# Kernel optimization log

Measured on AMD Instinct MI355X. Metric: run time of the kernel, lower is better.

Reference implementation:

```python
import jax, jax.numpy as jnp
import numpy as np

HEAD = 4
EPS = 1e-12


def _l2norm(x, axis):
    # torch F.normalize: x / max(||x||_2, eps)
    return x / jnp.maximum(jnp.linalg.norm(x, axis=axis, keepdims=True), EPS)


def setup_inputs() -> dict:
    key = jax.random.key(0)
    ks = jax.random.split(key, 12)
    n, t, c, h, w = 2, 7, 96, 96, 96
    inp = {
        "curr_feat": jax.random.normal(ks[0], (n, c, h, w), jnp.float32),
        "index_feat_set_s1": jax.random.normal(ks[1], (n, t, c, h, w), jnp.float32),
        "anchor_feat": jax.random.normal(ks[2], (n, c, h, w), jnp.float32),
        "sparse_feat_set_s1": jax.random.normal(ks[3], (n, t, c, h, w), jnp.float32),
        "sparse_feat_set_s2": jax.random.normal(ks[4], (n, t, c, h, w), jnp.float32),
        "sparse_feat_set_s3": jax.random.normal(ks[5], (n, t, c, h, w), jnp.float32),
        # absolute pixel coordinates (x,y interleaved per frame), mostly in-bounds
        # with a little overshoot to exercise zeros padding of grid_sample
        "location_feat": jax.random.uniform(ks[6], (n, t * 2, h, w), jnp.float32, minval=-2.0, maxval=float(w) + 1.0),
        "proj_w": 0.02 * jax.random.normal(ks[7], (c, c), jnp.float32),
        "proj_b": jnp.zeros((c,), jnp.float32),
        "fusion_w": 0.02 * jax.random.normal(ks[8], (c, 3 * c), jnp.float32),
        "fusion_b": jnp.zeros((c,), jnp.float32),
    }
    return inp


def reference(curr_feat, index_feat_set_s1, anchor_feat, sparse_feat_set_s1,
              sparse_feat_set_s2, sparse_feat_set_s3, location_feat,
              proj_w, proj_b, fusion_w, fusion_b):
    n, c, h, w = anchor_feat.shape
    t = sparse_feat_set_s1.shape[1]
    hd = c // HEAD
    hw = h * w

    # ---- flow-guided nearest grid_sample (align_corners=True, zeros pad) ----
    loc = location_feat.reshape(n, t, 2, h, w)  # (n,t,2,h,w): [x, y] pixel coords
    gx = 2.0 * loc[:, :, 0] / max(w - 1, 1) - 1.0
    gy = 2.0 * loc[:, :, 1] / max(h - 1, 1) - 1.0
    ix = jnp.round((gx + 1.0) * 0.5 * (w - 1))  # nearest (round-half-even, as torch)
    iy = jnp.round((gy + 1.0) * 0.5 * (h - 1))
    valid = (ix >= 0) & (ix <= w - 1) & (iy >= 0) & (iy <= h - 1)
    lin = (jnp.clip(iy, 0, h - 1).astype(jnp.int32) * w
           + jnp.clip(ix, 0, w - 1).astype(jnp.int32)).reshape(n, t, 1, hw)
    vmask = valid.reshape(n, t, 1, hw)

    def sample(f):  # f: (n,t,c,h,w) -> gathered (n,t,c,hw)
        g = jnp.take_along_axis(f.reshape(n, t, c, hw), lin, axis=3)
        return jnp.where(vmask, g, 0.0)

    samp1 = sample(sparse_feat_set_s1)
    samp2 = sample(sparse_feat_set_s2)
    samp3 = sample(sparse_feat_set_s3)
    sampi = sample(index_feat_set_s1)

    # ---- per-pixel multi-head max-correlation over t frames ----
    # queries: normalize over full channel dim c BEFORE splitting into heads
    q = _l2norm(curr_feat.reshape(n, c, hw).transpose(0, 2, 1), -1).reshape(n, hw, HEAD, hd)
    k = _l2norm(sampi.transpose(0, 3, 1, 2), -1).reshape(n, hw, t, HEAD, hd)
    scores = jnp.einsum('npthd,nphd->npht', k, q)  # scale == 1.0 in mode='max'
    corr_soft = jnp.max(scores, axis=3)     # (n,hw,head)
    corr_index = jnp.argmax(scores, axis=3)  # (n,hw,head), first-max like torch

    soft_img = jnp.broadcast_to(corr_soft[..., None], (n, hw, HEAD, hd)) \
                  .reshape(n, h, w, c).transpose(0, 3, 1, 2)  # (n,c,h,w)
    idx = jnp.broadcast_to(corr_index[..., None], (n, hw, HEAD, hd)) \
             .reshape(n, hw, c).transpose(0, 2, 1)[:, None]  # (n,1,c,hw)

    def pick(samp):  # select winning frame per (channel-group, pixel)
        return jnp.take_along_axis(samp, idx, axis=1)[:, 0].reshape(n, c, h, w)

    cat = jnp.concatenate([pick(samp1), pick(samp2), pick(samp3)], axis=1)  # (n,3c,h,w)
    out = jnp.einsum('ndhw,cd->nchw', cat, fusion_w) + fusion_b[None, :, None, None]
    out = out * soft_img
    out = jnp.einsum('nchw,dc->ndhw', out, proj_w) + proj_b[None, :, None, None]
    return out + anchor_feat
```

## Files before the change

### kernel.cpp

```cpp
#include <hip/hip_runtime.h>
#include <hip/hip_bf16.h>

#define N_    2
#define T_    7
#define C_    96
#define H_    96
#define W_    96
#define HW_   9216
#define HEAD_ 4
#define HD_   24
#define C3_   288
#define P_    16
#define QP_   100
#define CATP_ 292
#define NBLK_ (N_ * (HW_ / P_))
#define PLANES_ 14
#define CHUNK_  64
#define NCHUNK_ 144

typedef unsigned int u32;

__device__ __forceinline__ float bits2f(u32 b) {
    union { u32 u; float f; } x; x.u = b; return x.f;
}

__device__ __forceinline__ unsigned short f2bf(float f) {
    union { __hip_bfloat16 h; unsigned short s; } u;
    u.h = __float2bfloat16(f);
    return u.s;
}

template<bool BF16>
__device__ __forceinline__ float ld1(const void* p, int i) {
    if constexpr (BF16) return bits2f(((u32)((const unsigned short*)p)[i]) << 16);
    else                return ((const float*)p)[i];
}

template<bool BF16>
__device__ __forceinline__ void ld4w(const void* p, int i, float w[4]) {
    if constexpr (BF16) {
        const uint2 u = ((const uint2*)p)[i >> 2];
        w[0] = bits2f(u.x << 16);
        w[1] = bits2f(u.x & 0xFFFF0000u);
        w[2] = bits2f(u.y << 16);
        w[3] = bits2f(u.y & 0xFFFF0000u);
    } else {
        const float4 v = *((const float4*)((const float*)p + i));
        w[0] = v.x; w[1] = v.y; w[2] = v.z; w[3] = v.w;
    }
}

template<bool BF16>
__device__ __forceinline__ void st4w(void* p, int i, const float v[4]) {
    if constexpr (BF16) {
        uint2 w;
        w.x = (u32)f2bf(v[0]) | ((u32)f2bf(v[1]) << 16);
        w.y = (u32)f2bf(v[2]) | ((u32)f2bf(v[3]) << 16);
        ((uint2*)p)[i >> 2] = w;
    } else {
        *((float4*)((float*)p + i)) = make_float4(v[0], v[1], v[2], v[3]);
    }
}

__device__ __forceinline__ bool block_detect_bf16(const u32* __restrict__ w,
                                                  int tid, int* s_flag) {
    if (tid < 64) {
        u32 x = w[tid];
        u32 f = x & 0x7FFFu;
        int inwin = (f >= 0x3A00u) && (f <= 0x4200u);
        unsigned long long m = __ballot(inwin);
        if (tid == 0) *s_flag = (__popcll(m) >= 40) ? 1 : 0;
    }
    __syncthreads();
    return *s_flag != 0;
}

template<bool BF16>
__device__ __forceinline__ void transp_body(const void* __restrict__ src,
                                            void* __restrict__ dst,
                                            int bx, int tid, char* tileraw) {
    const int pl = bx / NCHUNK_;
    const int x0 = (bx - pl * NCHUNK_) * CHUNK_;
    if constexpr (BF16) {
        unsigned short (*tile)[CHUNK_ + 2] = (unsigned short (*)[CHUNK_ + 2])tileraw;
        const unsigned short* s = (const unsigned short*)src;
        unsigned short* d = (unsigned short*)dst;
        for (int i = tid; i < C_ * (CHUNK_ / 4); i += 256) {
            int ch = i >> 4, xq = i & 15;
            const ushort4 v = *((const ushort4*)(s + (pl * C_ + ch) * HW_ + x0 + 4 * xq));
            tile[ch][4 * xq + 0] = v.x; tile[ch][4 * xq + 1] = v.y;
            tile[ch][4 * xq + 2] = v.z; tile[ch][4 * xq + 3] = v.w;
        }
        __syncthreads();
        for (int i = tid; i < CHUNK_ * (C_ / 4); i += 256) {
            int p = i / 24, cq = i - p * 24;
            ushort4 v;
            v.x = tile[4 * cq + 0][p]; v.y = tile[4 * cq + 1][p];
            v.z = tile[4 * cq + 2][p]; v.w = tile[4 * cq + 3][p];
            *((ushort4*)(d + (pl * HW_ + x0 + p) * C_ + 4 * cq)) = v;
        }
    } else {
        float (*tile)[CHUNK_ + 1] = (float (*)[CHUNK_ + 1])tileraw;
        const float* s = (const float*)src;
        float* d = (float*)dst;
        for (int i = tid; i < C_ * (CHUNK_ / 4); i += 256) {
            int ch = i >> 4, xq = i & 15;
            const float4 v = *((const float4*)(s + (pl * C_ + ch) * HW_ + x0 + 4 * xq));
            tile[ch][4 * xq + 0] = v.x; tile[ch][4 * xq + 1] = v.y;
            tile[ch][4 * xq + 2] = v.z; tile[ch][4 * xq + 3] = v.w;
        }
        __syncthreads();
        for (int i = tid; i < CHUNK_ * (C_ / 4); i += 256) {
            int p = i / 24, cq = i - p * 24;
            float4 v;
            v.x = tile[4 * cq + 0][p]; v.y = tile[4 * cq + 1][p];
            v.z = tile[4 * cq + 2][p]; v.w = tile[4 * cq + 3][p];
            *((float4*)(d + (pl * HW_ + x0 + p) * C_ + 4 * cq)) = v;
        }
    }
}

__global__ __launch_bounds__(256) void transp_kernel(
    const void* __restrict__ idxf, void* __restrict__ dst,
    const u32* __restrict__ detect_src)
{
    __shared__ __align__(16) char tileraw[C_ * (CHUNK_ + 1) * 4];
    __shared__ int s_flag;
    const int tid = threadIdx.x;
    const bool bf = block_detect_bf16(detect_src, tid, &s_flag);
    if (bf) transp_body<true >(idxf, dst, blockIdx.x, tid, tileraw);
    else    transp_body<false>(idxf, dst, blockIdx.x, tid, tileraw);
}

template<bool BF16, int MODE>
__device__ __forceinline__ void traj_body(
    const void* __restrict__ curr, const void* __restrict__ idxf,
    const void* __restrict__ anchor, const void* __restrict__ s1,
    const void* __restrict__ s2, const void* __restrict__ s3,
    const void* __restrict__ loc, const void* __restrict__ pw,
    const void* __restrict__ pb, const void* __restrict__ fw,
    const void* __restrict__ fb, void* __restrict__ outp,
    const void* __restrict__ kT,
    float* s_u, float (*s_mid)[QP_], int (*s_lin)[P_], float (*s_red)[8],
    float (*s_best)[HEAD_], int (*s_bidx)[HEAD_], float* s_inv)
{
#define S_Q(pp, ch)  s_u[(pp) * QP_ + (ch)]
#define S_K(pp, ch)  s_u[P_ * QP_ + (pp) * QP_ + (ch)]
#define S_CAT(pp, d) s_u[(pp) * CATP_ + (d)]

    const int tid = threadIdx.x;
    const int b  = blockIdx.x;
    const int nn = b / (HW_ / P_);
    const int p0 = (b - nn * (HW_ / P_)) * P_;

    if (tid < T_ * P_) {
        int t = tid / P_, pp = tid - t * P_;
        int p = p0 + pp;
        float x = ld1<BF16>(loc, (nn * 2 * T_ + 2 * t    ) * HW_ + p);
        float y = ld1<BF16>(loc, (nn * 2 * T_ + 2 * t + 1) * HW_ + p);
        float gx = 2.0f * x / 95.0f - 1.0f;
        float gy = 2.0f * y / 95.0f - 1.0f;
        float fx = (gx + 1.0f) * 0.5f * 95.0f;
        float fy = (gy + 1.0f) * 0.5f * 95.0f;
        float ix = rintf(fx), iy = rintf(fy);
        bool v = (ix >= 0.0f) && (ix <= 95.0f) && (iy >= 0.0f) && (iy <= 95.0f);
        s_lin[t][pp] = v ? ((int)iy * W_ + (int)ix) : -1;
    }
    if (tid >= 128 && tid < 128 + P_ * HEAD_) {
        int q = tid - 128;
        s_best[q >> 2][q & 3] = -3.0e38f; s_bidx[q >> 2][q & 3] = 0;
    }

    for (int i = tid; i < C_ * (P_ / 4); i += 256) {
        int ch = i >> 2, pq = i & 3;
        float w[4];
        ld4w<BF16>(curr, (nn * C_ + ch) * HW_ + p0 + 4 * pq, w);
        S_Q(4 * pq + 0, ch) = w[0]; S_Q(4 * pq + 1, ch) = w[1];
        S_Q(4 * pq + 2, ch) = w[2]; S_Q(4 * pq + 3, ch) = w[3];
    }
    __syncthreads();

    if (tid < P_ * 8) {
        int pp = tid >> 3, j = tid & 7;
        float s = 0.f;
        #pragma unroll
        for (int k = 0; k < 12; ++k) { float v = S_Q(pp, j * 12 + k); s += v * v; }
        s_red[pp][j] = s;
    }
    __syncthreads();
    if (tid < P_) {
        float s = 0.f;
        #pragma unroll
        for (int j = 0; j < 8; ++j) s += s_red[tid][j];
        s_inv[tid] = 1.0f / fmaxf(sqrtf(s), 1e-12f);
    }
    __syncthreads();
    for (int i = tid; i < C_ * P_; i += 256) {
        int pp = i & (P_ - 1), ch = i >> 4;
        S_Q(pp, ch) *= s_inv[pp];
    }

    for (int t = 0; t < T_; ++t) {
        __syncthreads();
        if constexpr (MODE >= 1) {
            for (int i = tid; i < 24 * P_; i += 256) {
                int pp = i / 24, j = i - pp * 24;
                int lin = s_lin[t][pp];
                float w[4] = {0.f, 0.f, 0.f, 0.f};
                if (lin >= 0) ld4w<BF16>(kT, ((nn * T_ + t) * HW_ + lin) * C_ + 4 * j, w);
                *((float4*)&S_K(pp, 4 * j)) = make_float4(w[0], w[1], w[2], w[3]);
            }
        } else {
            for (int i = tid; i < C_ * P_; i += 256) {
                int ch = i / P_, pp = i - ch * P_;
                int lin = s_lin[t][pp];
                S_K(pp, ch) = (lin >= 0) ? ld1<BF16>(idxf, ((nn * T_ + t) * C_ + ch) * HW_ + lin) : 0.0f;
            }
        }
        __syncthreads();
        if (tid < P_ * 8) {
            int pp = tid >> 3, j = tid & 7;
            float s = 0.f;
            #pragma unroll
            for (int k = 0; k < 12; ++k) { float v = S_K(pp, j * 12 + k); s += v * v; }
            s_red[pp][j] = s;
        }
        __syncthreads();
        if (tid < P_) {
            float s = 0.f;
            #pragma unroll
            for (int j = 0; j < 8; ++j) s += s_red[tid][j];
            s_inv[tid] = 1.0f / fmaxf(sqrtf(s), 1e-12f);
        }
        __syncthreads();
        if (tid < P_ * HEAD_) {
            int pp = tid >> 2, h = tid & 3;
            float s = 0.f;
            #pragma unroll
            for (int dq = 0; dq < 6; ++dq) {
                const float4 kv = *((const float4*)&S_K(pp, h * HD_ + 4 * dq));
                const float4 qv = *((const float4*)&S_Q(pp, h * HD_ + 4 * dq));
                s += kv.x * qv.x; s += kv.y * qv.y; s += kv.z * qv.z; s += kv.w * qv.w;
            }
            s *= s_inv[pp];
            if (s > s_best[pp][h]) { s_best[pp][h] = s; s_bidx[pp][h] = t; }
        }
    }
    __syncthreads();

    for (int i = tid; i < C3_ * P_; i += 256) {
        int pp = i / C3_, d = i - pp * C3_;
        int set = d / C_, ch = d - set * C_;
        int h = ch / HD_;
        int bt = s_bidx[pp][h];
        int lin = s_lin[bt][pp];
        float v = 0.f;
        if (lin >= 0) {
            const void* sp = (set == 0) ? s1 : (set == 1) ? s2 : s3;
            v = ld1<BF16>(sp, ((nn * T_ + bt) * C_ + ch) * HW_ + lin);
        }
        S_CAT(pp, d) = v;
    }
    __syncthreads();

    if (tid < 96) {
        const int cq = tid >> 2, pq = tid & 3;
        const int co0 = cq * 4, px0 = pq * 4;
        float acc[4][4];
        #pragma unroll
        for (int r = 0; r < 4; ++r)
            #pragma unroll
            for (int k = 0; k < 4; ++k) acc[r][k] = 0.f;
        for (int d = 0; d < C3_; d += 4) {
            float4 cv[4];
            #pragma unroll
            for (int k = 0; k < 4; ++k) cv[k] = *((const float4*)&S_CAT(px0 + k, d));
            #pragma unroll
            for (int r = 0; r < 4; ++r) {
                float w[4]; ld4w<BF16>(fw, (co0 + r) * C3_ + d, w);
                #pragma unroll
                for (int k = 0; k < 4; ++k)
                    acc[r][k] += w[0] * cv[k].x + w[1] * cv[k].y + w[2] * cv[k].z + w[3] * cv[k].w;
            }
        }
        const int hh = co0 / HD_;
        #pragma unroll
        for (int r = 0; r < 4; ++r) {
            float fbv = ld1<BF16>(fb, co0 + r);
            #pragma unroll
            for (int k = 0; k < 4; ++k)
                s_mid[px0 + k][co0 + r] = (acc[r][k] + fbv) * s_best[px0 + k][hh];
        }
    }
    __syncthreads();

    if (tid < 96) {
        const int dq = tid >> 2, pq = tid & 3;
        const int do0 = dq * 4, px0 = pq * 4;
        float acc[4][4];
        #pragma unroll
        for (int r = 0; r < 4; ++r)
            #pragma unroll
            for (int k = 0; k < 4; ++k) acc[r][k] = 0.f;
        for (int c = 0; c < C_; c += 4) {
            float4 mv[4];
            #pragma unroll
            for (int k = 0; k < 4; ++k) mv[k] = *((const float4*)&s_mid[px0 + k][c]);
            #pragma unroll
            for (int r = 0; r < 4; ++r) {
                float w[4]; ld4w<BF16>(pw, (do0 + r) * C_ + c, w);
                #pragma unroll
                for (int k = 0; k < 4; ++k)
                    acc[r][k] += w[0] * mv[k].x + w[1] * mv[k].y + w[2] * mv[k].z + w[3] * mv[k].w;
            }
        }
        #pragma unroll
        for (int r = 0; r < 4; ++r) {
            float pbv = ld1<BF16>(pb, do0 + r);
            float av[4];
            ld4w<BF16>(anchor, (nn * C_ + do0 + r) * HW_ + p0 + px0, av);
            float res[4];
            #pragma unroll
            for (int k = 0; k < 4; ++k) res[k] = acc[r][k] + pbv + av[k];
            st4w<BF16>(outp, (nn * C_ + do0 + r) * HW_ + p0 + px0, res);
        }
    }
#undef S_Q
#undef S_K
#undef S_CAT
}

template<int MODE>
__global__ __launch_bounds__(256) void traj_main(
    const void* __restrict__ curr, const void* __restrict__ idxf,
    const void* __restrict__ anchor, const void* __restrict__ s1,
    const void* __restrict__ s2, const void* __restrict__ s3,
    const void* __restrict__ loc, const void* __restrict__ pw,
    const void* __restrict__ pb, const void* __restrict__ fw,
    const void* __restrict__ fb, void* __restrict__ outp,
    const void* __restrict__ kT)
{
    __shared__ __align__(16) float s_u[P_ * CATP_];
    __shared__ __align__(16) float s_mid[P_][QP_];
    __shared__ int   s_lin[T_][P_];
    __shared__ float s_red[P_][8];
    __shared__ float s_best[P_][HEAD_];
    __shared__ int   s_bidx[P_][HEAD_];
    __shared__ float s_inv[P_];
    __shared__ int   s_flag;

    const bool bf = block_detect_bf16((const u32*)curr, threadIdx.x, &s_flag);
    if (bf) traj_body<true,  MODE>(curr, idxf, anchor, s1, s2, s3, loc, pw, pb, fw, fb,
                                   outp, kT, s_u, s_mid, s_lin, s_red, s_best, s_bidx, s_inv);
    else    traj_body<false, MODE>(curr, idxf, anchor, s1, s2, s3, loc, pw, pb, fw, fb,
                                   outp, kT, s_u, s_mid, s_lin, s_red, s_best, s_bidx, s_inv);
}

extern "C" void kernel_launch(void* const* d_in, const int* in_sizes, int n_in,
                              void* d_out, int out_size, void* d_ws, size_t ws_size,
                              hipStream_t stream) {
    (void)in_sizes; (void)n_in; (void)out_size;
    const unsigned long long SZB = (unsigned long long)N_ * T_ * HW_ * C_ * 4ull;
    void* kT = d_ws;
    const int mode = (ws_size >= SZB) ? 1 : 0;

    dim3 grid(NBLK_), block(256);
    if (mode == 1) {
        transp_kernel<<<dim3(PLANES_ * NCHUNK_), 256, 0, stream>>>(d_in[1], kT, (const u32*)d_in[0]);
        traj_main<1><<<grid, block, 0, stream>>>(d_in[0], d_in[1], d_in[2], d_in[3], d_in[4],
                                                 d_in[5], d_in[6], d_in[7], d_in[8], d_in[9],
                                                 d_in[10], d_out, kT);
    } else {
        traj_main<0><<<grid, block, 0, stream>>>(d_in[0], d_in[1], d_in[2], d_in[3], d_in[4],
                                                 d_in[5], d_in[6], d_in[7], d_in[8], d_in[9],
                                                 d_in[10], d_out, kT);
    }
}
```

Measured before the change: 332.9 us.

## Gather all frames at once and restructure per-block work with 512 threads

The main kernel now loads the sampled key features for all seven frames in one batched phase instead of looping frame by frame with several barriers each. Norms, scores and the argmax are computed in parallel over frames and then reduced. The block size goes from 256 to 512 threads and the pixel tile from 16 to 12, with the fusion and projection matmuls remapped so each thread handles one pixel and four output channels. The goal is more memory-level parallelism and far fewer serialized barriers, at the cost of more shared memory per block and less register reuse of weights across pixels.

```diff
diff --git a/kernel.cpp b/kernel.cpp
--- a/kernel.cpp
+++ b/kernel.cpp
@@ -10,7 +10,7 @@
 #define HEAD_ 4
 #define HD_   24
 #define C3_   288
-#define P_    16
+#define P_    12
 #define QP_   100
 #define CATP_ 292
 #define NBLK_ (N_ * (HW_ / P_))
@@ -51,15 +51,9 @@
 }
 
 template<bool BF16>
-__device__ __forceinline__ void st4w(void* p, int i, const float v[4]) {
-    if constexpr (BF16) {
-        uint2 w;
-        w.x = (u32)f2bf(v[0]) | ((u32)f2bf(v[1]) << 16);
-        w.y = (u32)f2bf(v[2]) | ((u32)f2bf(v[3]) << 16);
-        ((uint2*)p)[i >> 2] = w;
-    } else {
-        *((float4*)((float*)p + i)) = make_float4(v[0], v[1], v[2], v[3]);
-    }
+__device__ __forceinline__ void st1(void* p, int i, float v) {
+    if constexpr (BF16) ((unsigned short*)p)[i] = f2bf(v);
+    else                ((float*)p)[i] = v;
 }
 
 __device__ __forceinline__ bool block_detect_bf16(const u32* __restrict__ w,
@@ -141,12 +135,13 @@
     const void* __restrict__ pb, const void* __restrict__ fw,
     const void* __restrict__ fb, void* __restrict__ outp,
     const void* __restrict__ kT,
-    float* s_u, float (*s_mid)[QP_], int (*s_lin)[P_], float (*s_red)[8],
-    float (*s_best)[HEAD_], int (*s_bidx)[HEAD_], float* s_inv)
+    float* s_q, float* s_ku, float (*s_mid)[QP_], int (*s_lin)[P_],
+    float* s_red, float* s_invq, float (*s_invk)[P_],
+    float (*s_score)[P_][HEAD_], float (*s_best)[HEAD_], int (*s_gbase)[HEAD_])
 {
-#define S_Q(pp, ch)  s_u[(pp) * QP_ + (ch)]
-#define S_K(pp, ch)  s_u[P_ * QP_ + (pp) * QP_ + (ch)]
-#define S_CAT(pp, d) s_u[(pp) * CATP_ + (d)]
+#define S_Q(pp, ch)     s_q[(pp) * QP_ + (ch)]
+#define S_K(t, pp, ch)  s_ku[((t) * P_ + (pp)) * QP_ + (ch)]
+#define S_CAT(pp, d)    s_ku[(pp) * CATP_ + (d)]
 
     const int tid = threadIdx.x;
     const int b  = blockIdx.x;
@@ -166,163 +161,160 @@
         bool v = (ix >= 0.0f) && (ix <= 95.0f) && (iy >= 0.0f) && (iy <= 95.0f);
         s_lin[t][pp] = v ? ((int)iy * W_ + (int)ix) : -1;
     }
-    if (tid >= 128 && tid < 128 + P_ * HEAD_) {
-        int q = tid - 128;
-        s_best[q >> 2][q & 3] = -3.0e38f; s_bidx[q >> 2][q & 3] = 0;
-    }
-
-    for (int i = tid; i < C_ * (P_ / 4); i += 256) {
-        int ch = i >> 2, pq = i & 3;
+    __syncthreads();
+
+    for (int i = tid; i < C_ * (P_ / 4); i += 512) {
+        int ch = i / (P_ / 4), pq = i - ch * (P_ / 4);
         float w[4];
         ld4w<BF16>(curr, (nn * C_ + ch) * HW_ + p0 + 4 * pq, w);
         S_Q(4 * pq + 0, ch) = w[0]; S_Q(4 * pq + 1, ch) = w[1];
         S_Q(4 * pq + 2, ch) = w[2]; S_Q(4 * pq + 3, ch) = w[3];
     }
-    __syncthreads();
-
-    if (tid < P_ * 8) {
-        int pp = tid >> 3, j = tid & 7;
+    if constexpr (MODE >= 1) {
+        for (int i = tid; i < T_ * P_ * 24; i += 512) {
+            int t = i / (P_ * 24), rem = i - t * (P_ * 24);
+            int pp = rem / 24, j = rem - pp * 24;
+            int lin = s_lin[t][pp];
+            float w[4] = {0.f, 0.f, 0.f, 0.f};
+            if (lin >= 0) ld4w<BF16>(kT, ((nn * T_ + t) * HW_ + lin) * C_ + 4 * j, w);
+            *((float4*)&S_K(t, pp, 4 * j)) = make_float4(w[0], w[1], w[2], w[3]);
+        }
+    } else {
+        for (int i = tid; i < T_ * C_ * P_; i += 512) {
+            int t = i / (C_ * P_), rem = i - t * (C_ * P_);
+            int ch = rem / P_, pp = rem - ch * P_;
+            int lin = s_lin[t][pp];
+            S_K(t, pp, ch) = (lin >= 0) ? ld1<BF16>(idxf, ((nn * T_ + t) * C_ + ch) * HW_ + lin) : 0.0f;
+        }
+    }
+    __syncthreads();
+
+    for (int i = tid; i < P_ * 8 + T_ * P_ * 8; i += 512) {
+        if (i < P_ * 8) {
+            int pp = i >> 3, j = i & 7;
+            float s = 0.f;
+            #pragma unroll
+            for (int k = 0; k < 12; ++k) { float v = S_Q(pp, j * 12 + k); s += v * v; }
+            s_red[pp * 8 + j] = s;
+        } else {
+            int idx = i - P_ * 8;
+            int t = idx / (P_ * 8), rem = idx - t * (P_ * 8);
+            int pp = rem >> 3, j = rem & 7;
+            float s = 0.f;
+            #pragma unroll
+            for (int k = 0; k < 12; ++k) { float v = S_K(t, pp, j * 12 + k); s += v * v; }
+            s_red[P_ * 8 + (t * P_ + pp) * 8 + j] = s;
+        }
+    }
+    __syncthreads();
+
+    if (tid < P_ + T_ * P_) {
+        if (tid < P_) {
+            float s = 0.f;
+            #pragma unroll
+            for (int j = 0; j < 8; ++j) s += s_red[tid * 8 + j];
+            s_invq[tid] = 1.0f / fmaxf(sqrtf(s), 1e-12f);
+        } else {
+            int idx = tid - P_;
+            int t = idx / P_, pp = idx - t * P_;
+            float s = 0.f;
+            #pragma unroll
+            for (int j = 0; j < 8; ++j) s += s_red[P_ * 8 + (t * P_ + pp) * 8 + j];
+            s_invk[t][pp] = 1.0f / fmaxf(sqrtf(s), 1e-12f);
+        }
+    }
+    __syncthreads();
+
+    for (int i = tid; i < P_ * 24; i += 512) {
+        int pp = i / 24, chq = i - pp * 24;
+        float4* p4 = (float4*)&S_Q(pp, 4 * chq);
+        float4 v = *p4;
+        float iv = s_invq[pp];
+        v.x *= iv; v.y *= iv; v.z *= iv; v.w *= iv;
+        *p4 = v;
+    }
+    __syncthreads();
+
+    for (int i = tid; i < T_ * P_ * HEAD_; i += 512) {
+        int t = i / (P_ * HEAD_), rem = i - t * (P_ * HEAD_);
+        int pp = rem >> 2, h = rem & 3;
         float s = 0.f;
         #pragma unroll
-        for (int k = 0; k < 12; ++k) { float v = S_Q(pp, j * 12 + k); s += v * v; }
-        s_red[pp][j] = s;
-    }
-    __syncthreads();
-    if (tid < P_) {
-        float s = 0.f;
+        for (int dq = 0; dq < 6; ++dq) {
+            const float4 kv = *((const float4*)&S_K(t, pp, h * HD_ + 4 * dq));
+            const float4 qv = *((const float4*)&S_Q(pp, h * HD_ + 4 * dq));
+            s += kv.x * qv.x; s += kv.y * qv.y; s += kv.z * qv.z; s += kv.w * qv.w;
+        }
+        s *= s_invk[t][pp];
+        s_score[t][pp][h] = s;
+    }
+    __syncthreads();
+
+    if (tid < P_ * HEAD_) {
+        int pp = tid >> 2, h = tid & 3;
+        float best = -3.0e38f; int bidx = 0;
         #pragma unroll
-        for (int j = 0; j < 8; ++j) s += s_red[tid][j];
-        s_inv[tid] = 1.0f / fmaxf(sqrtf(s), 1e-12f);
-    }
-    __syncthreads();
-    for (int i = tid; i < C_ * P_; i += 256) {
-        int pp = i & (P_ - 1), ch = i >> 4;
-        S_Q(pp, ch) *= s_inv[pp];
-    }
-
-    for (int t = 0; t < T_; ++t) {
-        __syncthreads();
-        if constexpr (MODE >= 1) {
-            for (int i = tid; i < 24 * P_; i += 256) {
-                int pp = i / 24, j = i - pp * 24;
-                int lin = s_lin[t][pp];
-                float w[4] = {0.f, 0.f, 0.f, 0.f};
-                if (lin >= 0) ld4w<BF16>(kT, ((nn * T_ + t) * HW_ + lin) * C_ + 4 * j, w);
-                *((float4*)&S_K(pp, 4 * j)) = make_float4(w[0], w[1], w[2], w[3]);
-            }
-        } else {
-            for (int i = tid; i < C_ * P_; i += 256) {
-                int ch = i / P_, pp = i - ch * P_;
-                int lin = s_lin[t][pp];
-                S_K(pp, ch) = (lin >= 0) ? ld1<BF16>(idxf, ((nn * T_ + t) * C_ + ch) * HW_ + lin) : 0.0f;
-            }
-        }
-        __syncthreads();
-        if (tid < P_ * 8) {
-            int pp = tid >> 3, j = tid & 7;
-            float s = 0.f;
-            #pragma unroll
-            for (int k = 0; k < 12; ++k) { float v = S_K(pp, j * 12 + k); s += v * v; }
-            s_red[pp][j] = s;
-        }
-        __syncthreads();
-        if (tid < P_) {
-            float s = 0.f;
-            #pragma unroll
-            for (int j = 0; j < 8; ++j) s += s_red[tid][j];
-            s_inv[tid] = 1.0f / fmaxf(sqrtf(s), 1e-12f);
-        }
-        __syncthreads();
-        if (tid < P_ * HEAD_) {
-            int pp = tid >> 2, h = tid & 3;
-            float s = 0.f;
-            #pragma unroll
-            for (int dq = 0; dq < 6; ++dq) {
-                const float4 kv = *((const float4*)&S_K(pp, h * HD_ + 4 * dq));
-                const float4 qv = *((const float4*)&S_Q(pp, h * HD_ + 4 * dq));
-                s += kv.x * qv.x; s += kv.y * qv.y; s += kv.z * qv.z; s += kv.w * qv.w;
-            }
-            s *= s_inv[pp];
-            if (s > s_best[pp][h]) { s_best[pp][h] = s; s_bidx[pp][h] = t; }
-        }
-    }
-    __syncthreads();
-
-    for (int i = tid; i < C3_ * P_; i += 256) {
+        for (int t = 0; t < T_; ++t) {
+            float v = s_score[t][pp][h];
+            if (v > best) { best = v; bidx = t; }
+        }
+        s_best[pp][h] = best;
+        int lin = s_lin[bidx][pp];
+        s_gbase[pp][h] = (lin >= 0) ? ((nn * T_ + bidx) * C_ * HW_ + lin) : -1;
+    }
+    __syncthreads();
+
+    for (int i = tid; i < C3_ * P_; i += 512) {
         int pp = i / C3_, d = i - pp * C3_;
         int set = d / C_, ch = d - set * C_;
-        int h = ch / HD_;
-        int bt = s_bidx[pp][h];
-        int lin = s_lin[bt][pp];
+        int gb = s_gbase[pp][ch / HD_];
         float v = 0.f;
-        if (lin >= 0) {
+        if (gb >= 0) {
             const void* sp = (set == 0) ? s1 : (set == 1) ? s2 : s3;
-            v = ld1<BF16>(sp, ((nn * T_ + bt) * C_ + ch) * HW_ + lin);
+            v = ld1<BF16>(sp, gb + ch * HW_);
         }
         S_CAT(pp, d) = v;
     }
     __syncthreads();
 
-    if (tid < 96) {
-        const int cq = tid >> 2, pq = tid & 3;
-        const int co0 = cq * 4, px0 = pq * 4;
-        float acc[4][4];
+    if (tid < 24 * P_) {
+        const int cq = tid / P_, px = tid - cq * P_;
+        const int co0 = cq * 4;
+        float acc[4] = {0.f, 0.f, 0.f, 0.f};
+        for (int d = 0; d < C3_; d += 4) {
+            const float4 cv = *((const float4*)&S_CAT(px, d));
+            #pragma unroll
+            for (int r = 0; r < 4; ++r) {
+                float w[4]; ld4w<BF16>(fw, (co0 + r) * C3_ + d, w);
+                acc[r] += w[0] * cv.x + w[1] * cv.y + w[2] * cv.z + w[3] * cv.w;
+            }
+        }
+        const int hh = co0 / HD_;
+        float soft = s_best[px][hh];
         #pragma unroll
         for (int r = 0; r < 4; ++r)
-            #pragma unroll
-            for (int k = 0; k < 4; ++k) acc[r][k] = 0.f;
-        for (int d = 0; d < C3_; d += 4) {
-            float4 cv[4];
-            #pragma unroll
-            for (int k = 0; k < 4; ++k) cv[k] = *((const float4*)&S_CAT(px0 + k, d));
+            s_mid[px][co0 + r] = (acc[r] + ld1<BF16>(fb, co0 + r)) * soft;
+    }
+    __syncthreads();
+
+    if (tid < 24 * P_) {
+        const int dq = tid / P_, px = tid - dq * P_;
+        const int do0 = dq * 4;
+        float acc[4] = {0.f, 0.f, 0.f, 0.f};
+        for (int c = 0; c < C_; c += 4) {
+            const float4 mv = *((const float4*)&s_mid[px][c]);
             #pragma unroll
             for (int r = 0; r < 4; ++r) {
-                float w[4]; ld4w<BF16>(fw, (co0 + r) * C3_ + d, w);
-                #pragma unroll
-                for (int k = 0; k < 4; ++k)
-                    acc[r][k] += w[0] * cv[k].x + w[1] * cv[k].y + w[2] * cv[k].z + w[3] * cv[k].w;
+                float w[4]; ld4w<BF16>(pw, (do0 + r) * C_ + c, w);
+                acc[r] += w[0] * mv.x + w[1] * mv.y + w[2] * mv.z + w[3] * mv.w;
             }
         }
-        const int hh = co0 / HD_;
+        int p = p0 + px;
         #pragma unroll
         for (int r = 0; r < 4; ++r) {
-            float fbv = ld1<BF16>(fb, co0 + r);
-            #pragma unroll
-            for (int k = 0; k < 4; ++k)
-                s_mid[px0 + k][co0 + r] = (acc[r][k] + fbv) * s_best[px0 + k][hh];
-        }
-    }
-    __syncthreads();
-
-    if (tid < 96) {
-        const int dq = tid >> 2, pq = tid & 3;
-        const int do0 = dq * 4, px0 = pq * 4;
-        float acc[4][4];
-        #pragma unroll
-        for (int r = 0; r < 4; ++r)
-            #pragma unroll
-            for (int k = 0; k < 4; ++k) acc[r][k] = 0.f;
-        for (int c = 0; c < C_; c += 4) {
-            float4 mv[4];
-            #pragma unroll
-            for (int k = 0; k < 4; ++k) mv[k] = *((const float4*)&s_mid[px0 + k][c]);
-            #pragma unroll
-            for (int r = 0; r < 4; ++r) {
-                float w[4]; ld4w<BF16>(pw, (do0 + r) * C_ + c, w);
-                #pragma unroll
-                for (int k = 0; k < 4; ++k)
-                    acc[r][k] += w[0] * mv[k].x + w[1] * mv[k].y + w[2] * mv[k].z + w[3] * mv[k].w;
-            }
-        }
-        #pragma unroll
-        for (int r = 0; r < 4; ++r) {
-            float pbv = ld1<BF16>(pb, do0 + r);
-            float av[4];
-            ld4w<BF16>(anchor, (nn * C_ + do0 + r) * HW_ + p0 + px0, av);
-            float res[4];
-            #pragma unroll
-            for (int k = 0; k < 4; ++k) res[k] = acc[r][k] + pbv + av[k];
-            st4w<BF16>(outp, (nn * C_ + do0 + r) * HW_ + p0 + px0, res);
+            float res = acc[r] + ld1<BF16>(pb, do0 + r)
+                      + ld1<BF16>(anchor, (nn * C_ + do0 + r) * HW_ + p);
+            st1<BF16>(outp, (nn * C_ + do0 + r) * HW_ + p, res);
         }
     }
 #undef S_Q
@@ -331,7 +323,7 @@
 }
 
 template<int MODE>
-__global__ __launch_bounds__(256) void traj_main(
+__global__ __launch_bounds__(512, 6) void traj_main(
     const void* __restrict__ curr, const void* __restrict__ idxf,
     const void* __restrict__ anchor, const void* __restrict__ s1,
     const void* __restrict__ s2, const void* __restrict__ s3,
@@ -340,20 +332,25 @@
     const void* __restrict__ fb, void* __restrict__ outp,
     const void* __restrict__ kT)
 {
-    __shared__ __align__(16) float s_u[P_ * CATP_];
+    __shared__ __align__(16) float s_q[P_ * QP_];
+    __shared__ __align__(16) float s_ku[T_ * P_ * QP_];
     __shared__ __align__(16) float s_mid[P_][QP_];
     __shared__ int   s_lin[T_][P_];
-    __shared__ float s_red[P_][8];
+    __shared__ float s_red[P_ * 8 + T_ * P_ * 8];
+    __shared__ float s_invq[P_];
+    __shared__ float s_invk[T_][P_];
+    __shared__ float s_score[T_][P_][HEAD_];
     __shared__ float s_best[P_][HEAD_];
-    __shared__ int   s_bidx[P_][HEAD_];
-    __shared__ float s_inv[P_];
+    __shared__ int   s_gbase[P_][HEAD_];
     __shared__ int   s_flag;
 
     const bool bf = block_detect_bf16((const u32*)curr, threadIdx.x, &s_flag);
     if (bf) traj_body<true,  MODE>(curr, idxf, anchor, s1, s2, s3, loc, pw, pb, fw, fb,
-                                   outp, kT, s_u, s_mid, s_lin, s_red, s_best, s_bidx, s_inv);
+                                   outp, kT, s_q, s_ku, s_mid, s_lin, s_red,
+                                   s_invq, s_invk, s_score, s_best, s_gbase);
     else    traj_body<false, MODE>(curr, idxf, anchor, s1, s2, s3, loc, pw, pb, fw, fb,
-                                   outp, kT, s_u, s_mid, s_lin, s_red, s_best, s_bidx, s_inv);
+                                   outp, kT, s_q, s_ku, s_mid, s_lin, s_red,
+                                   s_invq, s_invk, s_score, s_best, s_gbase);
 }
 
 extern "C" void kernel_launch(void* const* d_in, const int* in_sizes, int n_in,
@@ -364,7 +361,7 @@
     void* kT = d_ws;
     const int mode = (ws_size >= SZB) ? 1 : 0;
 
-    dim3 grid(NBLK_), block(256);
+    dim3 grid(NBLK_), block(512);
     if (mode == 1) {
         transp_kernel<<<dim3(PLANES_ * NCHUNK_), 256, 0, stream>>>(d_in[1], kT, (const u32*)d_in[0]);
         traj_main<1><<<grid, block, 0, stream>>>(d_in[0], d_in[1], d_in[2], d_in[3], d_in[4],
```

Result: slower. 398.6 us (+19.7%).

## Process frames in pairs and spread fusion/projection matmuls across all threads

Applied to the files above, without the earlier changes.

The frame loop now gathers and normalizes two key frames per iteration, which halves the number of barrier-separated phases, and the seventh frame is handled in a separate tail step. The running max and argmax are kept in registers, and a precomputed gather base offset replaces the per-element index lookup. The two small matmuls (fusion and projection) change from 96 threads computing 4x4 register tiles to all 256 threads computing one output each. This raises thread utilization but drops register reuse of the weights and activations, so weight loads per output go up. Shared memory for the s_u buffer grows to hold the two key frames.

```diff
diff --git a/kernel.cpp b/kernel.cpp
--- a/kernel.cpp
+++ b/kernel.cpp
@@ -51,15 +51,9 @@
 }
 
 template<bool BF16>
-__device__ __forceinline__ void st4w(void* p, int i, const float v[4]) {
-    if constexpr (BF16) {
-        uint2 w;
-        w.x = (u32)f2bf(v[0]) | ((u32)f2bf(v[1]) << 16);
-        w.y = (u32)f2bf(v[2]) | ((u32)f2bf(v[3]) << 16);
-        ((uint2*)p)[i >> 2] = w;
-    } else {
-        *((float4*)((float*)p + i)) = make_float4(v[0], v[1], v[2], v[3]);
-    }
+__device__ __forceinline__ void st1(void* p, int i, float v) {
+    if constexpr (BF16) ((unsigned short*)p)[i] = f2bf(v);
+    else                ((float*)p)[i] = v;
 }
 
 __device__ __forceinline__ bool block_detect_bf16(const u32* __restrict__ w,
@@ -141,12 +135,13 @@
     const void* __restrict__ pb, const void* __restrict__ fw,
     const void* __restrict__ fb, void* __restrict__ outp,
     const void* __restrict__ kT,
-    float* s_u, float (*s_mid)[QP_], int (*s_lin)[P_], float (*s_red)[8],
-    float (*s_best)[HEAD_], int (*s_bidx)[HEAD_], float* s_inv)
+    float* s_u, float (*s_mid)[QP_], int (*s_lin)[P_],
+    float (*s_red)[P_][8], float* s_invq, float (*s_invk)[P_],
+    float (*s_best)[HEAD_], int (*s_gbase)[HEAD_])
 {
-#define S_Q(pp, ch)  s_u[(pp) * QP_ + (ch)]
-#define S_K(pp, ch)  s_u[P_ * QP_ + (pp) * QP_ + (ch)]
-#define S_CAT(pp, d) s_u[(pp) * CATP_ + (d)]
+#define S_Q(pp, ch)      s_u[(pp) * QP_ + (ch)]
+#define S_KF(f, pp, ch)  s_u[P_ * QP_ + (f) * (P_ * QP_) + (pp) * QP_ + (ch)]
+#define S_CAT(pp, d)     s_u[(pp) * CATP_ + (d)]
 
     const int tid = threadIdx.x;
     const int b  = blockIdx.x;
@@ -166,10 +161,6 @@
         bool v = (ix >= 0.0f) && (ix <= 95.0f) && (iy >= 0.0f) && (iy <= 95.0f);
         s_lin[t][pp] = v ? ((int)iy * W_ + (int)ix) : -1;
     }
-    if (tid >= 128 && tid < 128 + P_ * HEAD_) {
-        int q = tid - 128;
-        s_best[q >> 2][q & 3] = -3.0e38f; s_bidx[q >> 2][q & 3] = 0;
-    }
 
     for (int i = tid; i < C_ * (P_ / 4); i += 256) {
         int ch = i >> 2, pq = i & 3;
@@ -185,148 +176,167 @@
         float s = 0.f;
         #pragma unroll
         for (int k = 0; k < 12; ++k) { float v = S_Q(pp, j * 12 + k); s += v * v; }
-        s_red[pp][j] = s;
+        s_red[0][pp][j] = s;
     }
     __syncthreads();
     if (tid < P_) {
         float s = 0.f;
         #pragma unroll
-        for (int j = 0; j < 8; ++j) s += s_red[tid][j];
-        s_inv[tid] = 1.0f / fmaxf(sqrtf(s), 1e-12f);
+        for (int j = 0; j < 8; ++j) s += s_red[0][tid][j];
+        s_invq[tid] = 1.0f / fmaxf(sqrtf(s), 1e-12f);
     }
     __syncthreads();
     for (int i = tid; i < C_ * P_; i += 256) {
         int pp = i & (P_ - 1), ch = i >> 4;
-        S_Q(pp, ch) *= s_inv[pp];
-    }
-
-    for (int t = 0; t < T_; ++t) {
+        S_Q(pp, ch) *= s_invq[pp];
+    }
+
+    float best = -3.0e38f; int bidx = 0;
+    const int dpp = tid >> 2, dh = tid & 3;
+
+    for (int tp = 0; tp < 3; ++tp) {
+        const int tA = 2 * tp;
         __syncthreads();
         if constexpr (MODE >= 1) {
-            for (int i = tid; i < 24 * P_; i += 256) {
-                int pp = i / 24, j = i - pp * 24;
-                int lin = s_lin[t][pp];
+            for (int i = tid; i < 2 * 24 * P_; i += 256) {
+                int f = i / (24 * P_), rem = i - f * (24 * P_);
+                int pp = rem / 24, j = rem - pp * 24;
+                int lin = s_lin[tA + f][pp];
                 float w[4] = {0.f, 0.f, 0.f, 0.f};
-                if (lin >= 0) ld4w<BF16>(kT, ((nn * T_ + t) * HW_ + lin) * C_ + 4 * j, w);
-                *((float4*)&S_K(pp, 4 * j)) = make_float4(w[0], w[1], w[2], w[3]);
+                if (lin >= 0) ld4w<BF16>(kT, ((nn * T_ + tA + f) * HW_ + lin) * C_ + 4 * j, w);
+                *((float4*)&S_KF(f, pp, 4 * j)) = make_float4(w[0], w[1], w[2], w[3]);
             }
         } else {
-            for (int i = tid; i < C_ * P_; i += 256) {
-                int ch = i / P_, pp = i - ch * P_;
-                int lin = s_lin[t][pp];
-                S_K(pp, ch) = (lin >= 0) ? ld1<BF16>(idxf, ((nn * T_ + t) * C_ + ch) * HW_ + lin) : 0.0f;
+            for (int i = tid; i < 2 * C_ * P_; i += 256) {
+                int f = i / (C_ * P_), rem = i - f * (C_ * P_);
+                int ch = rem / P_, pp = rem - ch * P_;
+                int lin = s_lin[tA + f][pp];
+                S_KF(f, pp, ch) = (lin >= 0)
+                    ? ld1<BF16>(idxf, ((nn * T_ + tA + f) * C_ + ch) * HW_ + lin) : 0.0f;
             }
         }
         __syncthreads();
-        if (tid < P_ * 8) {
-            int pp = tid >> 3, j = tid & 7;
+        {
+            int f = tid >> 7, rem = tid & 127;
+            int pp = rem >> 3, j = rem & 7;
             float s = 0.f;
             #pragma unroll
-            for (int k = 0; k < 12; ++k) { float v = S_K(pp, j * 12 + k); s += v * v; }
-            s_red[pp][j] = s;
-        }
-        __syncthreads();
-        if (tid < P_) {
+            for (int k = 0; k < 12; ++k) { float v = S_KF(f, pp, j * 12 + k); s += v * v; }
+            s_red[f][pp][j] = s;
+        }
+        __syncthreads();
+        if (tid < 2 * P_) {
+            int f = tid >> 4, pp = tid & 15;
             float s = 0.f;
             #pragma unroll
-            for (int j = 0; j < 8; ++j) s += s_red[tid][j];
-            s_inv[tid] = 1.0f / fmaxf(sqrtf(s), 1e-12f);
+            for (int j = 0; j < 8; ++j) s += s_red[f][pp][j];
+            s_invk[f][pp] = 1.0f / fmaxf(sqrtf(s), 1e-12f);
         }
         __syncthreads();
         if (tid < P_ * HEAD_) {
-            int pp = tid >> 2, h = tid & 3;
-            float s = 0.f;
             #pragma unroll
-            for (int dq = 0; dq < 6; ++dq) {
-                const float4 kv = *((const float4*)&S_K(pp, h * HD_ + 4 * dq));
-                const float4 qv = *((const float4*)&S_Q(pp, h * HD_ + 4 * dq));
-                s += kv.x * qv.x; s += kv.y * qv.y; s += kv.z * qv.z; s += kv.w * qv.w;
+            for (int f = 0; f < 2; ++f) {
+                float s = 0.f;
+                #pragma unroll
+                for (int dq = 0; dq < 6; ++dq) {
+                    const float4 kv = *((const float4*)&S_KF(f, dpp, dh * HD_ + 4 * dq));
+                    const float4 qv = *((const float4*)&S_Q(dpp, dh * HD_ + 4 * dq));
+                    s += kv.x * qv.x; s += kv.y * qv.y; s += kv.z * qv.z; s += kv.w * qv.w;
+                }
+                s *= s_invk[f][dpp];
+                if (s > best) { best = s; bidx = tA + f; }
             }
-            s *= s_inv[pp];
-            if (s > s_best[pp][h]) { s_best[pp][h] = s; s_bidx[pp][h] = t; }
-        }
+        }
+    }
+    __syncthreads();
+    if constexpr (MODE >= 1) {
+        for (int i = tid; i < 24 * P_; i += 256) {
+            int pp = i / 24, j = i - pp * 24;
+            int lin = s_lin[6][pp];
+            float w[4] = {0.f, 0.f, 0.f, 0.f};
+            if (lin >= 0) ld4w<BF16>(kT, ((nn * T_ + 6) * HW_ + lin) * C_ + 4 * j, w);
+            *((float4*)&S_KF(0, pp, 4 * j)) = make_float4(w[0], w[1], w[2], w[3]);
+        }
+    } else {
+        for (int i = tid; i < C_ * P_; i += 256) {
+            int ch = i / P_, pp = i - ch * P_;
+            int lin = s_lin[6][pp];
+            S_KF(0, pp, ch) = (lin >= 0)
+                ? ld1<BF16>(idxf, ((nn * T_ + 6) * C_ + ch) * HW_ + lin) : 0.0f;
+        }
+    }
+    __syncthreads();
+    if (tid < P_ * 8) {
+        int pp = tid >> 3, j = tid & 7;
+        float s = 0.f;
+        #pragma unroll
+        for (int k = 0; k < 12; ++k) { float v = S_KF(0, pp, j * 12 + k); s += v * v; }
+        s_red[0][pp][j] = s;
+    }
+    __syncthreads();
+    if (tid < P_) {
+        float s = 0.f;
+        #pragma unroll
+        for (int j = 0; j < 8; ++j) s += s_red[0][tid][j];
+        s_invk[0][tid] = 1.0f / fmaxf(sqrtf(s), 1e-12f);
+    }
+    __syncthreads();
+    if (tid < P_ * HEAD_) {
+        float s = 0.f;
+        #pragma unroll
+        for (int dq = 0; dq < 6; ++dq) {
+            const float4 kv = *((const float4*)&S_KF(0, dpp, dh * HD_ + 4 * dq));
+            const float4 qv = *((const float4*)&S_Q(dpp, dh * HD_ + 4 * dq));
+            s += kv.x * qv.x; s += kv.y * qv.y; s += kv.z * qv.z; s += kv.w * qv.w;
+        }
+        s *= s_invk[0][dpp];
+        if (s > best) { best = s; bidx = 6; }
+        s_best[dpp][dh] = best;
+        int lin = s_lin[bidx][dpp];
+        s_gbase[dpp][dh] = (lin >= 0) ? ((nn * T_ + bidx) * C_ * HW_ + lin) : -1;
     }
     __syncthreads();
 
     for (int i = tid; i < C3_ * P_; i += 256) {
         int pp = i / C3_, d = i - pp * C3_;
         int set = d / C_, ch = d - set * C_;
-        int h = ch / HD_;
-        int bt = s_bidx[pp][h];
-        int lin = s_lin[bt][pp];
+        int gb = s_gbase[pp][ch / HD_];
         float v = 0.f;
-        if (lin >= 0) {
+        if (gb >= 0) {
             const void* sp = (set == 0) ? s1 : (set == 1) ? s2 : s3;
-            v = ld1<BF16>(sp, ((nn * T_ + bt) * C_ + ch) * HW_ + lin);
+            v = ld1<BF16>(sp, gb + ch * HW_);
         }
         S_CAT(pp, d) = v;
     }
     __syncthreads();
 
-    if (tid < 96) {
-        const int cq = tid >> 2, pq = tid & 3;
-        const int co0 = cq * 4, px0 = pq * 4;
-        float acc[4][4];
-        #pragma unroll
-        for (int r = 0; r < 4; ++r)
-            #pragma unroll
-            for (int k = 0; k < 4; ++k) acc[r][k] = 0.f;
+    for (int u = tid; u < C_ * P_; u += 256) {
+        int co = u >> 4, px = u & 15;
+        float acc = 0.f;
         for (int d = 0; d < C3_; d += 4) {
-            float4 cv[4];
-            #pragma unroll
-            for (int k = 0; k < 4; ++k) cv[k] = *((const float4*)&S_CAT(px0 + k, d));
-            #pragma unroll
-            for (int r = 0; r < 4; ++r) {
-                float w[4]; ld4w<BF16>(fw, (co0 + r) * C3_ + d, w);
-                #pragma unroll
-                for (int k = 0; k < 4; ++k)
-                    acc[r][k] += w[0] * cv[k].x + w[1] * cv[k].y + w[2] * cv[k].z + w[3] * cv[k].w;
-            }
-        }
-        const int hh = co0 / HD_;
-        #pragma unroll
-        for (int r = 0; r < 4; ++r) {
-            float fbv = ld1<BF16>(fb, co0 + r);
-            #pragma unroll
-            for (int k = 0; k < 4; ++k)
-                s_mid[px0 + k][co0 + r] = (acc[r][k] + fbv) * s_best[px0 + k][hh];
-        }
-    }
-    __syncthreads();
-
-    if (tid < 96) {
-        const int dq = tid >> 2, pq = tid & 3;
-        const int do0 = dq * 4, px0 = pq * 4;
-        float acc[4][4];
-        #pragma unroll
-        for (int r = 0; r < 4; ++r)
-            #pragma unroll
-            for (int k = 0; k < 4; ++k) acc[r][k] = 0.f;
+            float w[4]; ld4w<BF16>(fw, co * C3_ + d, w);
+            const float4 cv = *((const float4*)&S_CAT(px, d));
+            acc += w[0] * cv.x + w[1] * cv.y + w[2] * cv.z + w[3] * cv.w;
+        }
+        s_mid[px][co] = (acc + ld1<BF16>(fb, co)) * s_best[px][co / HD_];
+    }
+    __syncthreads();
+
+    for (int u = tid; u < C_ * P_; u += 256) {
+        int dd = u >> 4, px = u & 15;
+        float acc = 0.f;
         for (int c = 0; c < C_; c += 4) {
-            float4 mv[4];
-            #pragma unroll
-            for (int k = 0; k < 4; ++k) mv[k] = *((const float4*)&s_mid[px0 + k][c]);
-            #pragma unroll
-            for (int r = 0; r < 4; ++r) {
-                float w[4]; ld4w<BF16>(pw, (do0 + r) * C_ + c, w);
-                #pragma unroll
-                for (int k = 0; k < 4; ++k)
-                    acc[r][k] += w[0] * mv[k].x + w[1] * mv[k].y + w[2] * mv[k].z + w[3] * mv[k].w;
-            }
-        }
-        #pragma unroll
-        for (int r = 0; r < 4; ++r) {
-            float pbv = ld1<BF16>(pb, do0 + r);
-            float av[4];
-            ld4w<BF16>(anchor, (nn * C_ + do0 + r) * HW_ + p0 + px0, av);
-            float res[4];
-            #pragma unroll
-            for (int k = 0; k < 4; ++k) res[k] = acc[r][k] + pbv + av[k];
-            st4w<BF16>(outp, (nn * C_ + do0 + r) * HW_ + p0 + px0, res);
-        }
+            float w[4]; ld4w<BF16>(pw, dd * C_ + c, w);
+            const float4 mv = *((const float4*)&s_mid[px][c]);
+            acc += w[0] * mv.x + w[1] * mv.y + w[2] * mv.z + w[3] * mv.w;
+        }
+        int p = p0 + px;
+        float res = acc + ld1<BF16>(pb, dd)
+                  + ld1<BF16>(anchor, (nn * C_ + dd) * HW_ + p);
+        st1<BF16>(outp, (nn * C_ + dd) * HW_ + p, res);
     }
 #undef S_Q
-#undef S_K
+#undef S_KF
 #undef S_CAT
 }
 
@@ -340,20 +350,23 @@
     const void* __restrict__ fb, void* __restrict__ outp,
     const void* __restrict__ kT)
 {
-    __shared__ __align__(16) float s_u[P_ * CATP_];
+    __shared__ __align__(16) float s_u[3 * P_ * QP_];
     __shared__ __align__(16) float s_mid[P_][QP_];
     __shared__ int   s_lin[T_][P_];
-    __shared__ float s_red[P_][8];
+    __shared__ float s_red[2][P_][8];
+    __shared__ float s_invq[P_];
+    __shared__ float s_invk[2][P_];
     __shared__ float s_best[P_][HEAD_];
-    __shared__ int   s_bidx[P_][HEAD_];
-    __shared__ float s_inv[P_];
+    __shared__ int   s_gbase[P_][HEAD_];
     __shared__ int   s_flag;
 
     const bool bf = block_detect_bf16((const u32*)curr, threadIdx.x, &s_flag);
     if (bf) traj_body<true,  MODE>(curr, idxf, anchor, s1, s2, s3, loc, pw, pb, fw, fb,
-                                   outp, kT, s_u, s_mid, s_lin, s_red, s_best, s_bidx, s_inv);
+                                   outp, kT, s_u, s_mid, s_lin, s_red, s_invq,
+                                   s_invk, s_best, s_gbase);
     else    traj_body<false, MODE>(curr, idxf, anchor, s1, s2, s3, loc, pw, pb, fw, fb,
-                                   outp, kT, s_u, s_mid, s_lin, s_red, s_best, s_bidx, s_inv);
+                                   outp, kT, s_u, s_mid, s_lin, s_red, s_invq,
+                                   s_invk, s_best, s_gbase);
 }
 
 extern "C" void kernel_launch(void* const* d_in, const int* in_sizes, int n_in,
```

Result: slower. 381.2 us (+14.5%).
